# Performance work log

Measured on AMD Instinct MI355X. Metric: run time of the kernel, lower is better.

Reference implementation:

```python
import jax, jax.numpy as jnp
import numpy as np

N_NODES = 100000
N_EDGES = 3200000
F_IN, HID, N_CLS = 512, 16, 40


def setup_inputs() -> dict:
    key = jax.random.key(0)
    ks = jax.random.split(key, 7)
    x = jax.random.normal(ks[0], (N_NODES, F_IN), dtype=jnp.float32)
    edge_index = jax.random.randint(ks[1], (2, N_EDGES), 0, N_NODES, dtype=jnp.int32)
    edge_weight = jax.random.uniform(ks[2], (N_EDGES,), dtype=jnp.float32)
    # Glorot-style init like PyG's Linear inside GCNConv
    W1 = jax.random.normal(ks[3], (F_IN, HID), dtype=jnp.float32) * (1.0 / np.sqrt(F_IN))
    b1 = jnp.zeros((HID,), dtype=jnp.float32)
    W2 = jax.random.normal(ks[4], (HID, N_CLS), dtype=jnp.float32) * (1.0 / np.sqrt(HID))
    b2 = jnp.zeros((N_CLS,), dtype=jnp.float32)
    return {"x": x, "edge_index": edge_index, "edge_weight": edge_weight,
            "W1": W1, "b1": b1, "W2": W2, "b2": b2}


def reference(x, edge_index, edge_weight, W1, b1, W2, b2):
    N = x.shape[0]
    src, dst = edge_index[0], edge_index[1]
    # add self-loops with weight 1 (GCNConv default add_self_loops=True)
    loop = jnp.arange(N, dtype=edge_index.dtype)
    src_f = jnp.concatenate([src, loop])
    dst_f = jnp.concatenate([dst, loop])
    ew_f = jnp.concatenate([edge_weight, jnp.ones((N,), dtype=edge_weight.dtype)])
    # symmetric normalization: deg computed over target nodes (source_to_target flow)
    deg = jax.ops.segment_sum(ew_f, dst_f, num_segments=N)
    dis = jnp.where(deg > 0, jax.lax.rsqrt(jnp.where(deg > 0, deg, 1.0)), 0.0)
    norm = dis[src_f] * ew_f * dis[dst_f]  # [E+N]

    def conv(h, W, b):
        h = h @ W  # linear before propagate, as in PyG GCNConv
        msg = h[src_f] * norm[:, None]  # [E+N, d_out]
        agg = jax.ops.segment_sum(msg, dst_f, num_segments=N)
        return agg + b

    h = jax.nn.relu(conv(x, W1, b1))
    # dropout is identity in eval mode
    out = conv(h, W2, b2)
    return jax.nn.log_softmax(out, axis=1)
```

## Files before the change

### kernel.cpp

```cpp
#include <hip/hip_runtime.h>
#include <hip/hip_bf16.h>

constexpr int F_IN  = 512;
constexpr int HID   = 16;
constexpr int NCLS  = 40;
constexpr int CHUNK = 4096;
constexpr int BMAX  = 800;
constexpr int SMAX  = 6144;

__device__ __forceinline__ unsigned packEdge(int s, float w) {
  __hip_bfloat16 h = __float2bfloat16(w);
  unsigned short hb = *reinterpret_cast<unsigned short*>(&h);
  return ((unsigned)s << 15) | (unsigned)(hb & 0x7fff);
}
__device__ __forceinline__ float edgeW(unsigned p) {
  return __uint_as_float((p & 0x7fffu) << 16);
}

__global__ void k_zpad(int* __restrict__ counts, int lo, int hi) {
  int i = lo + blockIdx.x * 256 + threadIdx.x;
  if (i < hi) counts[i] = 0;
}

__global__ void k_scanA(const int* __restrict__ a, int* __restrict__ bsum) {
  __shared__ int sd[256];
  int t = threadIdx.x;
  int4 v = reinterpret_cast<const int4*>(a)[blockIdx.x * 256 + t];
  sd[t] = v.x + v.y + v.z + v.w;
  __syncthreads();
  for (int off = 128; off > 0; off >>= 1) {
    if (t < off) sd[t] += sd[t + off];
    __syncthreads();
  }
  if (!t) bsum[blockIdx.x] = sd[0];
}

__global__ void k_scanB(int* __restrict__ bsum, int nb) {
  __shared__ int sd[1024];
  int t = threadIdx.x;
  int v = (t < nb) ? bsum[t] : 0;
  sd[t] = v;
  __syncthreads();
  for (int off = 1; off < 1024; off <<= 1) {
    int add = (t >= off) ? sd[t - off] : 0;
    __syncthreads();
    sd[t] += add;
    __syncthreads();
  }
  if (t < nb) bsum[t] = sd[t] - v;
}

__global__ void k_scanC(int* __restrict__ a, const int* __restrict__ bsum) {
  __shared__ int sd[256];
  int t = threadIdx.x;
  int4 v = reinterpret_cast<int4*>(a)[blockIdx.x * 256 + t];
  int ts = v.x + v.y + v.z + v.w;
  sd[t] = ts;
  __syncthreads();
  for (int off = 1; off < 256; off <<= 1) {
    int add = (t >= off) ? sd[t - off] : 0;
    __syncthreads();
    sd[t] += add;
    __syncthreads();
  }
  int pre = bsum[blockIdx.x] + sd[t] - ts;
  int4 w;
  w.x = pre; w.y = pre + v.x; w.z = w.y + v.y; w.w = w.z + v.z;
  reinterpret_cast<int4*>(a)[blockIdx.x * 256 + t] = w;
}

__global__ void __launch_bounds__(256)
k_scat2(const int* __restrict__ src, const int* __restrict__ dst,
        const float* __restrict__ ew, unsigned* __restrict__ payloadA,
        unsigned char* __restrict__ dlowA, int* __restrict__ segs,
        int* __restrict__ counts, int E, int NB, int NBLK) {
  __shared__ unsigned ebuf32[CHUNK];
  __shared__ unsigned char ebufd[CHUNK];
  __shared__ int hist[1024];
  __shared__ int sc[256];
  int t = threadIdx.x;
  int c = blockIdx.x;
  int cbase = c * CHUNK;
  int sz = min(CHUNK, E - cbase);
#pragma unroll
  for (int i = 0; i < 4; ++i) hist[t + 256 * i] = 0;
  __syncthreads();
  unsigned pk[16];
  unsigned char dl[16];
  int key[16];
#pragma unroll
  for (int r = 0; r < 16; ++r) {
    int i = r * 256 + t;
    int e = cbase + i;
    if (i < sz) {
      int s = src[e], d = dst[e];
      pk[r] = packEdge(s, ew[e]);
      dl[r] = (unsigned char)(d & 127);
      key[r] = d >> 7;
      atomicAdd(&hist[key[r]], 1);
    } else {
      key[r] = -1;
    }
  }
  __syncthreads();
  int h0 = hist[4 * t], h1 = hist[4 * t + 1], h2 = hist[4 * t + 2], h3 = hist[4 * t + 3];
  int tsum = h0 + h1 + h2 + h3;
  sc[t] = tsum;
  __syncthreads();
  for (int off = 1; off < 256; off <<= 1) {
    int add = (t >= off) ? sc[t - off] : 0;
    __syncthreads();
    sc[t] += add;
    __syncthreads();
  }
  int pre = sc[t] - tsum;
  __syncthreads();
  hist[4 * t]     = pre;
  hist[4 * t + 1] = pre + h0;
  hist[4 * t + 2] = pre + h0 + h1;
  hist[4 * t + 3] = pre + h0 + h1 + h2;
  __syncthreads();
  size_t sb = (size_t)c * (NB + 1);
  for (int b = t; b < NB; b += 256) {
    int lo = hist[b];
    segs[sb + b] = lo;
    counts[b * NBLK + c] = hist[b + 1] - lo;
  }
  if (t == 0) segs[sb + NB] = sz;
  __syncthreads();
#pragma unroll
  for (int r = 0; r < 16; ++r) {
    if (key[r] >= 0) {
      int pos = atomicAdd(&hist[key[r]], 1);
      ebuf32[pos] = pk[r];
      ebufd[pos]  = dl[r];
    }
  }
  __syncthreads();
  for (int i = t; i < sz; i += 256) {
    payloadA[cbase + i] = ebuf32[i];
    dlowA[cbase + i]    = ebufd[i];
  }
}

__global__ void __launch_bounds__(256)
k_sortb2(const unsigned* __restrict__ payloadA, const unsigned char* __restrict__ dlowA,
         const int* __restrict__ segs, const int* __restrict__ cnts,
         unsigned* __restrict__ payloadB, int* __restrict__ rs,
         float* __restrict__ dis, int N, int NB, int NBLK) {
  __shared__ unsigned ebuf32[SMAX];
  __shared__ unsigned char ebufd[SMAX];
  __shared__ int hcnt[128];
  __shared__ int scn[128];
  __shared__ float dgs[128];
  int t = threadIdx.x;
  int b = blockIdx.x;
  if (t < 128) { hcnt[t] = 0; dgs[t] = 1.0f; }
  __syncthreads();
  int beg = cnts[b * NBLK];
  int end = cnts[b * NBLK + NBLK];
  for (int c = t; c < NBLK; c += 256) {
    int rel = cnts[b * NBLK + c] - beg;
    size_t sb = (size_t)c * (NB + 1) + b;
    int s0 = segs[sb], s1 = segs[sb + 1];
    int gsrc = c * CHUNK + s0;
    for (int k = 0; k < s1 - s0; ++k) {
      unsigned p = payloadA[gsrc + k];
      unsigned char d8 = dlowA[gsrc + k];
      ebuf32[rel + k] = p;
      ebufd[rel + k]  = d8;
      atomicAdd(&hcnt[d8], 1);
      atomicAdd(&dgs[d8], edgeW(p));
    }
  }
  __syncthreads();
  int v = (t < 128) ? hcnt[t] : 0;
  if (t < 128) scn[t] = v;
  __syncthreads();
  for (int off = 1; off < 128; off <<= 1) {
    int add = (t < 128 && t >= off) ? scn[t - off] : 0;
    __syncthreads();
    if (t < 128) scn[t] += add;
    __syncthreads();
  }
  int base = b * 128;
  if (t < 128) {
    int st = scn[t] - v;
    hcnt[t] = st;
    rs[base + t] = beg + st;
    int n = base + t;
    if (n < N) dis[n] = rsqrtf(dgs[t]);
  }
  if (t == 0) rs[base + 128] = end;
  __syncthreads();
  int sz = end - beg;
  for (int i = t; i < sz; i += 256) {
    int pos = beg + atomicAdd(&hcnt[ebufd[i]], 1);
    payloadB[pos] = ebuf32[i];
  }
}

__device__ __forceinline__ float blo(unsigned u) { return __uint_as_float(u << 16); }
__device__ __forceinline__ float bhi(unsigned u) { return __uint_as_float(u & 0xffff0000u); }
__device__ __forceinline__ unsigned pack2(float lo, float hi) {
  __hip_bfloat16 l = __float2bfloat16(lo), h = __float2bfloat16(hi);
  unsigned short ul = *reinterpret_cast<unsigned short*>(&l);
  unsigned short uh = *reinterpret_cast<unsigned short*>(&h);
  return (unsigned)ul | ((unsigned)uh << 16);
}

__global__ void __launch_bounds__(256)
k_gemm1f(const float* __restrict__ x, const float* __restrict__ W1,
         const float* __restrict__ dis, uint4* __restrict__ hb1, int N) {
  __shared__ unsigned xs[4352];
  int t = threadIdx.x;
  int nb = blockIdx.x * 64;
  int r = t & 63;
  int sId = __builtin_amdgcn_readfirstlane(t >> 6);
  float2 acc[8];
#pragma unroll
  for (int j2 = 0; j2 < 8; ++j2) acc[j2] = make_float2(0.f, 0.f);

  float4 ld0, ld1, ld2, ld3, ld4, ld5, ld6, ld7;
#define G1F_LOAD(c)                                                          \
  do {                                                                       \
    int f;                                                                   \
    f = t;           { int row = f >> 5, sl = f & 31; int n = nb + row;      \
      ld0 = (n < N) ? *reinterpret_cast<const float4*>(x + (size_t)n * F_IN + (c) * 128 + sl * 4) : make_float4(0,0,0,0); } \
    f = t + 256;     { int row = f >> 5, sl = f & 31; int n = nb + row;      \
      ld1 = (n < N) ? *reinterpret_cast<const float4*>(x + (size_t)n * F_IN + (c) * 128 + sl * 4) : make_float4(0,0,0,0); } \
    f = t + 512;     { int row = f >> 5, sl = f & 31; int n = nb + row;      \
      ld2 = (n < N) ? *reinterpret_cast<const float4*>(x + (size_t)n * F_IN + (c) * 128 + sl * 4) : make_float4(0,0,0,0); } \
    f = t + 768;     { int row = f >> 5, sl = f & 31; int n = nb + row;      \
      ld3 = (n < N) ? *reinterpret_cast<const float4*>(x + (size_t)n * F_IN + (c) * 128 + sl * 4) : make_float4(0,0,0,0); } \
    f = t + 1024;    { int row = f >> 5, sl = f & 31; int n = nb + row;      \
      ld4 = (n < N) ? *reinterpret_cast<const float4*>(x + (size_t)n * F_IN + (c) * 128 + sl * 4) : make_float4(0,0,0,0); } \
    f = t + 1280;    { int row = f >> 5, sl = f & 31; int n = nb + row;      \
      ld5 = (n < N) ? *reinterpret_cast<const float4*>(x + (size_t)n * F_IN + (c) * 128 + sl * 4) : make_float4(0,0,0,0); } \
    f = t + 1536;    { int row = f >> 5, sl = f & 31; int n = nb + row;      \
      ld6 = (n < N) ? *reinterpret_cast<const float4*>(x + (size_t)n * F_IN + (c) * 128 + sl * 4) : make_float4(0,0,0,0); } \
    f = t + 1792;    { int row = f >> 5, sl = f & 31; int n = nb + row;      \
      ld7 = (n < N) ? *reinterpret_cast<const float4*>(x + (size_t)n * F_IN + (c) * 128 + sl * 4) : make_float4(0,0,0,0); } \
  } while (0)
#define G1F_STORE()                                                          \
  do {                                                                       \
    int f;                                                                   \
    f = t;        { int row = f >> 5, sl = f & 31; int w = row * 65 + sl * 2; \
      xs[w] = pack2(ld0.x, ld0.y); xs[w + 1] = pack2(ld0.z, ld0.w); }        \
    f = t + 256;  { int row = f >> 5, sl = f & 31; int w = row * 65 + sl * 2; \
      xs[w] = pack2(ld1.x, ld1.y); xs[w + 1] = pack2(ld1.z, ld1.w); }        \
    f = t + 512;  { int row = f >> 5, sl = f & 31; int w = row * 65 + sl * 2; \
      xs[w] = pack2(ld2.x, ld2.y); xs[w + 1] = pack2(ld2.z, ld2.w); }        \
    f = t + 768;  { int row = f >> 5, sl = f & 31; int w = row * 65 + sl * 2; \
      xs[w] = pack2(ld3.x, ld3.y); xs[w + 1] = pack2(ld3.z, ld3.w); }        \
    f = t + 1024; { int row = f >> 5, sl = f & 31; int w = row * 65 + sl * 2; \
      xs[w] = pack2(ld4.x, ld4.y); xs[w + 1] = pack2(ld4.z, ld4.w); }        \
    f = t + 1280; { int row = f >> 5, sl = f & 31; int w = row * 65 + sl * 2; \
      xs[w] = pack2(ld5.x, ld5.y); xs[w + 1] = pack2(ld5.z, ld5.w); }        \
    f = t + 1536; { int row = f >> 5, sl = f & 31; int w = row * 65 + sl * 2; \
      xs[w] = pack2(ld6.x, ld6.y); xs[w + 1] = pack2(ld6.z, ld6.w); }        \
    f = t + 1792; { int row = f >> 5, sl = f & 31; int w = row * 65 + sl * 2; \
      xs[w] = pack2(ld7.x, ld7.y); xs[w + 1] = pack2(ld7.z, ld7.w); }        \
  } while (0)

  G1F_LOAD(0);

#pragma unroll
  for (int c = 0; c < 4; ++c) {
    __syncthreads();
    G1F_STORE();
    if (c < 3) G1F_LOAD(c + 1);
    __syncthreads();
    {
      const unsigned* xcol = &xs[r * 65 + sId * 16];
      const float* wbase = W1 + (size_t)(c * 128 + sId * 32) * HID;
#pragma unroll
      for (int mm = 0; mm < 16; ++mm) {
        unsigned u = xcol[mm];
        float x0 = blo(u), x1 = bhi(u);
        const float* w0 = wbase + mm * 32;
        const float* w1 = w0 + HID;
#pragma unroll
        for (int j2 = 0; j2 < 8; ++j2) {
          float2 p0 = *reinterpret_cast<const float2*>(w0 + 2 * j2);
          float2 p1 = *reinterpret_cast<const float2*>(w1 + 2 * j2);
          acc[j2].x = fmaf(x1, p1.x, fmaf(x0, p0.x, acc[j2].x));
          acc[j2].y = fmaf(x1, p1.y, fmaf(x0, p0.y, acc[j2].y));
        }
      }
    }
  }

  __syncthreads();
  float* ps = reinterpret_cast<float*>(xs);
#pragma unroll
  for (int j2 = 0; j2 < 8; ++j2) {
    ps[(sId * 64 + r) * 17 + 2 * j2]     = acc[j2].x;
    ps[(sId * 64 + r) * 17 + 2 * j2 + 1] = acc[j2].y;
  }
  __syncthreads();
  if (t < 64) {
    int n = nb + t;
    if (n < N) {
      float di = dis[n];
      float o[HID];
#pragma unroll
      for (int j = 0; j < HID; ++j)
        o[j] = (ps[t * 17 + j] + ps[(64 + t) * 17 + j] +
                ps[(128 + t) * 17 + j] + ps[(192 + t) * 17 + j]) * di;
      uint4 w0, w1;
      w0.x = pack2(o[0],  o[1]);  w0.y = pack2(o[2],  o[3]);
      w0.z = pack2(o[4],  o[5]);  w0.w = pack2(o[6],  o[7]);
      w1.x = pack2(o[8],  o[9]);  w1.y = pack2(o[10], o[11]);
      w1.z = pack2(o[12], o[13]); w1.w = pack2(o[14], o[15]);
      hb1[(size_t)n * 2]     = w0;
      hb1[(size_t)n * 2 + 1] = w1;
    }
  }
#undef G1F_LOAD
#undef G1F_STORE
}

template <int LAYER>
__global__ void __launch_bounds__(256)
k_aggn4(const unsigned* __restrict__ payload, const int* __restrict__ rs,
        const uint4* __restrict__ hb, const float* __restrict__ dis,
        const float* __restrict__ b1, uint4* __restrict__ hb2,
        const float* __restrict__ W2, const float* __restrict__ b2,
        float* __restrict__ out, int N) {
  int tid = blockIdx.x * 256 + threadIdx.x;
  int n = tid >> 2;
  int q = tid & 3;
  if (n >= N) return;
  int e0 = rs[n], e1 = rs[n + 1];
  float a0 = 0, a1 = 0, a2 = 0, a3 = 0, a4 = 0, a5 = 0, a6 = 0, a7 = 0;
  float a8 = 0, a9 = 0, a10 = 0, a11 = 0, a12 = 0, a13 = 0, a14 = 0, a15 = 0;
  for (int e = e0 + q; e < e1; e += 4) {
    unsigned p = payload[e];
    const uint4* row = hb + ((size_t)(p >> 15) * 2);
    uint4 r0 = row[0];
    uint4 r1 = row[1];
    float w = edgeW(p);
    a0  = fmaf(blo(r0.x), w, a0);  a1  = fmaf(bhi(r0.x), w, a1);
    a2  = fmaf(blo(r0.y), w, a2);  a3  = fmaf(bhi(r0.y), w, a3);
    a4  = fmaf(blo(r0.z), w, a4);  a5  = fmaf(bhi(r0.z), w, a5);
    a6  = fmaf(blo(r0.w), w, a6);  a7  = fmaf(bhi(r0.w), w, a7);
    a8  = fmaf(blo(r1.x), w, a8);  a9  = fmaf(bhi(r1.x), w, a9);
    a10 = fmaf(blo(r1.y), w, a10); a11 = fmaf(bhi(r1.y), w, a11);
    a12 = fmaf(blo(r1.z), w, a12); a13 = fmaf(bhi(r1.z), w, a13);
    a14 = fmaf(blo(r1.w), w, a14); a15 = fmaf(bhi(r1.w), w, a15);
  }
#pragma unroll
  for (int m = 1; m <= 2; m <<= 1) {
    a0  += __shfl_xor(a0,  m); a1  += __shfl_xor(a1,  m);
    a2  += __shfl_xor(a2,  m); a3  += __shfl_xor(a3,  m);
    a4  += __shfl_xor(a4,  m); a5  += __shfl_xor(a5,  m);
    a6  += __shfl_xor(a6,  m); a7  += __shfl_xor(a7,  m);
    a8  += __shfl_xor(a8,  m); a9  += __shfl_xor(a9,  m);
    a10 += __shfl_xor(a10, m); a11 += __shfl_xor(a11, m);
    a12 += __shfl_xor(a12, m); a13 += __shfl_xor(a13, m);
    a14 += __shfl_xor(a14, m); a15 += __shfl_xor(a15, m);
  }
  uint4 s0 = hb[(size_t)n * 2];
  uint4 s1 = hb[(size_t)n * 2 + 1];
  float di = dis[n];
  a0  = (a0  + blo(s0.x)) * di;  a1  = (a1  + bhi(s0.x)) * di;
  a2  = (a2  + blo(s0.y)) * di;  a3  = (a3  + bhi(s0.y)) * di;
  a4  = (a4  + blo(s0.z)) * di;  a5  = (a5  + bhi(s0.z)) * di;
  a6  = (a6  + blo(s0.w)) * di;  a7  = (a7  + bhi(s0.w)) * di;
  a8  = (a8  + blo(s1.x)) * di;  a9  = (a9  + bhi(s1.x)) * di;
  a10 = (a10 + blo(s1.y)) * di;  a11 = (a11 + bhi(s1.y)) * di;
  a12 = (a12 + blo(s1.z)) * di;  a13 = (a13 + bhi(s1.z)) * di;
  a14 = (a14 + blo(s1.w)) * di;  a15 = (a15 + bhi(s1.w)) * di;
  if (LAYER == 1) {
    a0  = fmaxf(a0  + b1[0],  0.0f) * di;  a1  = fmaxf(a1  + b1[1],  0.0f) * di;
    a2  = fmaxf(a2  + b1[2],  0.0f) * di;  a3  = fmaxf(a3  + b1[3],  0.0f) * di;
    a4  = fmaxf(a4  + b1[4],  0.0f) * di;  a5  = fmaxf(a5  + b1[5],  0.0f) * di;
    a6  = fmaxf(a6  + b1[6],  0.0f) * di;  a7  = fmaxf(a7  + b1[7],  0.0f) * di;
    a8  = fmaxf(a8  + b1[8],  0.0f) * di;  a9  = fmaxf(a9  + b1[9],  0.0f) * di;
    a10 = fmaxf(a10 + b1[10], 0.0f) * di;  a11 = fmaxf(a11 + b1[11], 0.0f) * di;
    a12 = fmaxf(a12 + b1[12], 0.0f) * di;  a13 = fmaxf(a13 + b1[13], 0.0f) * di;
    a14 = fmaxf(a14 + b1[14], 0.0f) * di;  a15 = fmaxf(a15 + b1[15], 0.0f) * di;
    if (q == 0) {
      uint4 w0;
      w0.x = pack2(a0, a1);  w0.y = pack2(a2,  a3);
      w0.z = pack2(a4, a5);  w0.w = pack2(a6,  a7);
      hb2[(size_t)n * 2] = w0;
    } else if (q == 1) {
      uint4 w1;
      w1.x = pack2(a8,  a9);  w1.y = pack2(a10, a11);
      w1.z = pack2(a12, a13); w1.w = pack2(a14, a15);
      hb2[(size_t)n * 2 + 1] = w1;
    }
  } else {
    float gv[16] = {a0, a1, a2, a3, a4, a5, a6, a7,
                    a8, a9, a10, a11, a12, a13, a14, a15};
    float o[10];
#pragma unroll
    for (int cc = 0; cc < 10; ++cc) o[cc] = b2[q * 10 + cc];
#pragma unroll
    for (int j = 0; j < HID; ++j) {
      float gj = gv[j];
      const float* wr = W2 + j * NCLS + q * 10;
#pragma unroll
      for (int cc = 0; cc < 10; ++cc) o[cc] = fmaf(gj, wr[cc], o[cc]);
    }
    float m = o[0];
#pragma unroll
    for (int cc = 1; cc < 10; ++cc) m = fmaxf(m, o[cc]);
    m = fmaxf(m, __shfl_xor(m, 1));
    m = fmaxf(m, __shfl_xor(m, 2));
    float ss = 0.0f;
#pragma unroll
    for (int cc = 0; cc < 10; ++cc) ss += expf(o[cc] - m);
    ss += __shfl_xor(ss, 1);
    ss += __shfl_xor(ss, 2);
    float lse = m + logf(ss);
    float* orow = out + (size_t)n * NCLS + q * 10;
#pragma unroll
    for (int cc = 0; cc < 10; ++cc) orow[cc] = o[cc] - lse;
  }
}

extern "C" void kernel_launch(void* const* d_in, const int* in_sizes, int n_in,
                              void* d_out, int out_size, void* d_ws, size_t ws_size,
                              hipStream_t stream) {
  const float* x  = (const float*)d_in[0];
  const int*   ei = (const int*)d_in[1];
  const float* ew = (const float*)d_in[2];
  const float* W1 = (const float*)d_in[3];
  const float* b1 = (const float*)d_in[4];
  const float* W2 = (const float*)d_in[5];
  const float* b2 = (const float*)d_in[6];
  float* out = (float*)d_out;

  const int N = in_sizes[0] / F_IN;
  const int E = in_sizes[2];
  const int* src = ei;
  const int* dst = ei + E;

  const int NB   = (N + 127) >> 7;
  const int NBLK = (E + CHUNK - 1) / CHUNK;
  const long long SCT = (long long)NB * NBLK + 1;
  const int Npad = (int)((SCT + 1023) & ~1023LL);
  const int nbScan = Npad / 1024;
  const int Nr   = (NB * 128 + 256 + 255) & ~255;
  const size_t SEGSZ = (size_t)NBLK * (NB + 1) + 4;

  int* counts = (int*)d_ws;
  int* bsum   = counts + Npad;
  float* dis  = (float*)(bsum + 1024);
  int* rs     = (int*)(dis + Nr);
  uint4* hb1  = (uint4*)(rs + Nr);
  uint4* hb2  = hb1 + (size_t)N * 2;
  unsigned* payloadA = (unsigned*)(hb2 + (size_t)N * 2);
  unsigned char* dlowA = (unsigned char*)(payloadA + (size_t)E);
  int* segs   = (int*)(dlowA + (((size_t)E + 3) & ~3ull));
  unsigned* payloadB = (unsigned*)(segs + SEGSZ);

  const int padLo = NB * NBLK;
  k_zpad<<<(Npad - padLo + 255) / 256, 256, 0, stream>>>(counts, padLo, Npad);
  k_scat2<<<NBLK, 256, 0, stream>>>(src, dst, ew, payloadA, dlowA, segs, counts, E, NB, NBLK);
  k_scanA<<<nbScan, 256, 0, stream>>>(counts, bsum);
  k_scanB<<<1, 1024, 0, stream>>>(bsum, nbScan);
  k_scanC<<<nbScan, 256, 0, stream>>>(counts, bsum);
  k_sortb2<<<NB, 256, 0, stream>>>(payloadA, dlowA, segs, counts, payloadB, rs, dis, N, NB, NBLK);
  k_gemm1f<<<(N + 63) / 64, 256, 0, stream>>>(x, W1, dis, hb1, N);
  const int gAgg = (N * 4 + 255) / 256;
  k_aggn4<1><<<gAgg, 256, 0, stream>>>(payloadB, rs, hb1, dis, b1, hb2,
                                       nullptr, nullptr, nullptr, N);
  k_aggn4<2><<<gAgg, 256, 0, stream>>>(payloadB, rs, hb2, dis, nullptr, nullptr,
                                       W2, b2, out, N);
}
```

Measured before the change: 227.0 us.

## Replace LDS-staged bf16 GEMM1 with direct per-thread nontemporal row reads

The first-layer GEMM no longer stages x tiles through shared memory as bf16 with double-buffered loads. Each thread now streams its own 128-float slice of a node row straight from global memory with nontemporal float4 loads and accumulates in fp32. This removes the LDS round trip, the barriers and the bf16 conversion, and slightly improves precision. The cost is uncoalesced access, since each lane reads a different 2KB-strided row, which may hurt DRAM efficiency on the 200MB x read.

```diff
diff --git a/kernel.cpp b/kernel.cpp
--- a/kernel.cpp
+++ b/kernel.cpp
@@ -7,6 +7,8 @@
 constexpr int CHUNK = 4096;
 constexpr int BMAX  = 800;
 constexpr int SMAX  = 6144;
+
+typedef float f4v __attribute__((ext_vector_type(4)));
 
 __device__ __forceinline__ unsigned packEdge(int s, float w) {
   __hip_bfloat16 h = __float2bfloat16(w);
@@ -210,97 +212,36 @@
 }
 
 __global__ void __launch_bounds__(256)
-k_gemm1f(const float* __restrict__ x, const float* __restrict__ W1,
+k_gemm1g(const float* __restrict__ x, const float* __restrict__ W1,
          const float* __restrict__ dis, uint4* __restrict__ hb1, int N) {
-  __shared__ unsigned xs[4352];
-  int t = threadIdx.x;
+  __shared__ float ps[4 * 64 * 17];
+  int t = threadIdx.x;
+  int r = t & 63, s = t >> 6;
   int nb = blockIdx.x * 64;
-  int r = t & 63;
-  int sId = __builtin_amdgcn_readfirstlane(t >> 6);
-  float2 acc[8];
-#pragma unroll
-  for (int j2 = 0; j2 < 8; ++j2) acc[j2] = make_float2(0.f, 0.f);
-
-  float4 ld0, ld1, ld2, ld3, ld4, ld5, ld6, ld7;
-#define G1F_LOAD(c)                                                          \
-  do {                                                                       \
-    int f;                                                                   \
-    f = t;           { int row = f >> 5, sl = f & 31; int n = nb + row;      \
-      ld0 = (n < N) ? *reinterpret_cast<const float4*>(x + (size_t)n * F_IN + (c) * 128 + sl * 4) : make_float4(0,0,0,0); } \
-    f = t + 256;     { int row = f >> 5, sl = f & 31; int n = nb + row;      \
-      ld1 = (n < N) ? *reinterpret_cast<const float4*>(x + (size_t)n * F_IN + (c) * 128 + sl * 4) : make_float4(0,0,0,0); } \
-    f = t + 512;     { int row = f >> 5, sl = f & 31; int n = nb + row;      \
-      ld2 = (n < N) ? *reinterpret_cast<const float4*>(x + (size_t)n * F_IN + (c) * 128 + sl * 4) : make_float4(0,0,0,0); } \
-    f = t + 768;     { int row = f >> 5, sl = f & 31; int n = nb + row;      \
-      ld3 = (n < N) ? *reinterpret_cast<const float4*>(x + (size_t)n * F_IN + (c) * 128 + sl * 4) : make_float4(0,0,0,0); } \
-    f = t + 1024;    { int row = f >> 5, sl = f & 31; int n = nb + row;      \
-      ld4 = (n < N) ? *reinterpret_cast<const float4*>(x + (size_t)n * F_IN + (c) * 128 + sl * 4) : make_float4(0,0,0,0); } \
-    f = t + 1280;    { int row = f >> 5, sl = f & 31; int n = nb + row;      \
-      ld5 = (n < N) ? *reinterpret_cast<const float4*>(x + (size_t)n * F_IN + (c) * 128 + sl * 4) : make_float4(0,0,0,0); } \
-    f = t + 1536;    { int row = f >> 5, sl = f & 31; int n = nb + row;      \
-      ld6 = (n < N) ? *reinterpret_cast<const float4*>(x + (size_t)n * F_IN + (c) * 128 + sl * 4) : make_float4(0,0,0,0); } \
-    f = t + 1792;    { int row = f >> 5, sl = f & 31; int n = nb + row;      \
-      ld7 = (n < N) ? *reinterpret_cast<const float4*>(x + (size_t)n * F_IN + (c) * 128 + sl * 4) : make_float4(0,0,0,0); } \
-  } while (0)
-#define G1F_STORE()                                                          \
-  do {                                                                       \
-    int f;                                                                   \
-    f = t;        { int row = f >> 5, sl = f & 31; int w = row * 65 + sl * 2; \
-      xs[w] = pack2(ld0.x, ld0.y); xs[w + 1] = pack2(ld0.z, ld0.w); }        \
-    f = t + 256;  { int row = f >> 5, sl = f & 31; int w = row * 65 + sl * 2; \
-      xs[w] = pack2(ld1.x, ld1.y); xs[w + 1] = pack2(ld1.z, ld1.w); }        \
-    f = t + 512;  { int row = f >> 5, sl = f & 31; int w = row * 65 + sl * 2; \
-      xs[w] = pack2(ld2.x, ld2.y); xs[w + 1] = pack2(ld2.z, ld2.w); }        \
-    f = t + 768;  { int row = f >> 5, sl = f & 31; int w = row * 65 + sl * 2; \
-      xs[w] = pack2(ld3.x, ld3.y); xs[w + 1] = pack2(ld3.z, ld3.w); }        \
-    f = t + 1024; { int row = f >> 5, sl = f & 31; int w = row * 65 + sl * 2; \
-      xs[w] = pack2(ld4.x, ld4.y); xs[w + 1] = pack2(ld4.z, ld4.w); }        \
-    f = t + 1280; { int row = f >> 5, sl = f & 31; int w = row * 65 + sl * 2; \
-      xs[w] = pack2(ld5.x, ld5.y); xs[w + 1] = pack2(ld5.z, ld5.w); }        \
-    f = t + 1536; { int row = f >> 5, sl = f & 31; int w = row * 65 + sl * 2; \
-      xs[w] = pack2(ld6.x, ld6.y); xs[w + 1] = pack2(ld6.z, ld6.w); }        \
-    f = t + 1792; { int row = f >> 5, sl = f & 31; int w = row * 65 + sl * 2; \
-      xs[w] = pack2(ld7.x, ld7.y); xs[w + 1] = pack2(ld7.z, ld7.w); }        \
-  } while (0)
-
-  G1F_LOAD(0);
-
-#pragma unroll
-  for (int c = 0; c < 4; ++c) {
-    __syncthreads();
-    G1F_STORE();
-    if (c < 3) G1F_LOAD(c + 1);
-    __syncthreads();
-    {
-      const unsigned* xcol = &xs[r * 65 + sId * 16];
-      const float* wbase = W1 + (size_t)(c * 128 + sId * 32) * HID;
-#pragma unroll
-      for (int mm = 0; mm < 16; ++mm) {
-        unsigned u = xcol[mm];
-        float x0 = blo(u), x1 = bhi(u);
-        const float* w0 = wbase + mm * 32;
-        const float* w1 = w0 + HID;
-#pragma unroll
-        for (int j2 = 0; j2 < 8; ++j2) {
-          float2 p0 = *reinterpret_cast<const float2*>(w0 + 2 * j2);
-          float2 p1 = *reinterpret_cast<const float2*>(w1 + 2 * j2);
-          acc[j2].x = fmaf(x1, p1.x, fmaf(x0, p0.x, acc[j2].x));
-          acc[j2].y = fmaf(x1, p1.y, fmaf(x0, p0.y, acc[j2].y));
-        }
+  int n = nb + r;
+  float acc[HID];
+#pragma unroll
+  for (int j = 0; j < HID; ++j) acc[j] = 0.0f;
+  if (n < N) {
+    const f4v* xr = reinterpret_cast<const f4v*>(x + (size_t)n * F_IN + s * 128);
+    const float* wp = W1 + (size_t)(s * 128) * HID;
+#pragma unroll 8
+    for (int c = 0; c < 32; ++c) {
+      f4v v = __builtin_nontemporal_load(xr + c);
+      const float* wr = wp + (c * 4) * HID;
+#pragma unroll
+      for (int j = 0; j < HID; ++j) {
+        acc[j] = fmaf(v.x, wr[j], acc[j]);
+        acc[j] = fmaf(v.y, wr[HID + j], acc[j]);
+        acc[j] = fmaf(v.z, wr[2 * HID + j], acc[j]);
+        acc[j] = fmaf(v.w, wr[3 * HID + j], acc[j]);
       }
     }
   }
-
-  __syncthreads();
-  float* ps = reinterpret_cast<float*>(xs);
-#pragma unroll
-  for (int j2 = 0; j2 < 8; ++j2) {
-    ps[(sId * 64 + r) * 17 + 2 * j2]     = acc[j2].x;
-    ps[(sId * 64 + r) * 17 + 2 * j2 + 1] = acc[j2].y;
-  }
+#pragma unroll
+  for (int j = 0; j < HID; ++j) ps[(s * 64 + r) * 17 + j] = acc[j];
   __syncthreads();
   if (t < 64) {
-    int n = nb + t;
     if (n < N) {
       float di = dis[n];
       float o[HID];
@@ -317,8 +258,6 @@
       hb1[(size_t)n * 2 + 1] = w1;
     }
   }
-#undef G1F_LOAD
-#undef G1F_STORE
 }
 
 template <int LAYER>
@@ -465,7 +404,7 @@
   k_scanB<<<1, 1024, 0, stream>>>(bsum, nbScan);
   k_scanC<<<nbScan, 256, 0, stream>>>(counts, bsum);
   k_sortb2<<<NB, 256, 0, stream>>>(payloadA, dlowA, segs, counts, payloadB, rs, dis, N, NB, NBLK);
-  k_gemm1f<<<(N + 63) / 64, 256, 0, stream>>>(x, W1, dis, hb1, N);
+  k_gemm1g<<<(N + 63) / 64, 256, 0, stream>>>(x, W1, dis, hb1, N);
   const int gAgg = (N * 4 + 255) / 256;
   k_aggn4<1><<<gAgg, 256, 0, stream>>>(payloadB, rs, hb1, dis, b1, hb2,
                                        nullptr, nullptr, nullptr, N);
```

Measured after the change: 377.6 us. +66.3%, slower.
